# Kernel tuning notes

Measured on AMD Instinct MI355X. Metric: run time of the kernel, lower is better.

## Reference

```python
import jax, jax.numpy as jnp
import numpy as np

NU = 50000   # n_users
NI = 50000   # n_items
N = NU + NI  # total nodes in the square normalized adjacency
D = 64       # emb_dim
K = 4        # number of sub-graphs in hypergraph_list
E = 1000000  # interactions per sub-graph (symmetrized -> 2E nnz)


def setup_inputs() -> dict:
    key = jax.random.key(0)
    ks = jax.random.split(key, 9)
    stdv = 1.0 / np.sqrt(D)
    return {
        "x": jax.random.normal(ks[0], (N, D), jnp.float32),
        "hgc1_bias": jax.random.uniform(ks[1], (D,), jnp.float32, -stdv, stdv),
        "fc1_W": jax.random.normal(ks[2], (D, D), jnp.float32) * stdv,
        "fus_l1_W": jax.random.normal(ks[3], (D, D), jnp.float32) * stdv,
        "fus_l1_b": jnp.zeros((D,), jnp.float32),
        "fus_l2_W": jax.random.normal(ks[4], (1, D), jnp.float32) * stdv,
        "fus_l2_b": jnp.zeros((1,), jnp.float32),
        "rows": jax.random.randint(ks[5], (K, E), 0, NU),
        "cols": jax.random.randint(ks[6], (K, E), 0, NI),
    }


def reference(x, hgc1_bias, fc1_W, fus_l1_W, fus_l1_b, fus_l2_W, fus_l2_b, rows, cols):
    def spmm(src, dst, val, h):
        # (L @ h)[i] = sum over nnz (src=i): val * h[dst]
        return jax.ops.segment_sum(val[:, None] * h[dst], src, num_segments=N)

    def step(xc, rc):
        r, c = rc
        # symmetric bipartite adjacency A (items offset by NU)
        src = jnp.concatenate([r, c + NU])  # (2E,)
        dst = jnp.concatenate([c + NU, r])  # (2E,)
        # D^-1/2 A D^-1/2  (degree = row nnz count, as in (A>0).sum)
        deg = jax.ops.segment_sum(jnp.ones(src.shape, jnp.float32), src, num_segments=N) + 1e-7
        dinv = deg ** -0.5
        val = dinv[src] * dinv[dst]
        # HGNN2: relu -> hgc1 (bias add, edge=G^T x, x=G edge; G symmetric) -> softmax -> fc1
        h = jax.nn.relu(xc) + hgc1_bias
        edge = spmm(src, dst, val, h)
        node = spmm(src, dst, val, edge)
        node = jax.nn.softmax(node, axis=1)
        node = node @ fc1_W.T  # fc1 has no bias
        # Fusion gate (dropout off in eval)
        emb = jnp.stack([xc, node])  # (2, N, D)
        score = jax.nn.softmax(
            jnp.tanh(emb @ fus_l1_W.T + fus_l1_b) @ fus_l2_W.T + fus_l2_b, axis=0
        )  # (2, N, 1)
        x_new = jnp.sum(score * emb, axis=0)
        return x_new, (x_new, edge)

    _, (nodes, edges) = jax.lax.scan(step, x, (rows, cols))
    # embedding_list[sub_key] = [x, edge] per sub-graph -> stacked (K, N, D)
    return nodes, edges
```

## Files before the change

### kernel.cpp

```cpp
#include <hip/hip_runtime.h>
#include <hip/hip_bf16.h>

#define NU_ 50000
#define NI_ 50000
#define NN  (NU_ + NI_)
#define DD  64
#define KK  4
#define EE  1000000
#define SCAN_B ((NN + 255) / 256)

#define P_RANGES 8
#define RANGE_SZ ((NN + P_RANGES - 1) / P_RANGES)

__global__ void k_hist(const int* __restrict__ r, const int* __restrict__ c,
                       int* __restrict__ cnt) {
    int e = blockIdx.x * blockDim.x + threadIdx.x;
    if (e >= EE) return;
    int a = r[e], b = c[e];
    if ((unsigned)a >= (unsigned)NU_ || (unsigned)b >= (unsigned)NI_) return;
    atomicAdd(&cnt[a], 1);
    atomicAdd(&cnt[NU_ + b], 1);
}

__global__ __launch_bounds__(256) void k_bsum(const int* __restrict__ cnt,
                                              int* __restrict__ bsum) {
    __shared__ int s[256];
    int i = blockIdx.x * 256 + threadIdx.x;
    s[threadIdx.x] = (i < NN) ? cnt[i] : 0;
    __syncthreads();
    #pragma unroll
    for (int off = 128; off > 0; off >>= 1) {
        if (threadIdx.x < off) s[threadIdx.x] += s[threadIdx.x + off];
        __syncthreads();
    }
    if (threadIdx.x == 0) bsum[blockIdx.x] = s[0];
}

__global__ __launch_bounds__(512) void k_sscan(const int* __restrict__ bsum,
                                               int* __restrict__ bofs) {
    __shared__ int s[512];
    int tid = threadIdx.x;
    s[tid] = (tid < SCAN_B) ? bsum[tid] : 0;
    __syncthreads();
    #pragma unroll
    for (int off = 1; off < 512; off <<= 1) {
        int v = (tid >= off) ? s[tid - off] : 0;
        __syncthreads();
        s[tid] += v;
        __syncthreads();
    }
    if (tid < SCAN_B) bofs[tid] = (tid > 0) ? s[tid - 1] : 0;
}

__global__ __launch_bounds__(256) void k_apply(const int* __restrict__ cnt,
                                               const int* __restrict__ bofs,
                                               int* __restrict__ row_ptr,
                                               int* __restrict__ cursor,
                                               float* __restrict__ dinv) {
    __shared__ int s[256];
    int i = blockIdx.x * 256 + threadIdx.x;
    int v = (i < NN) ? cnt[i] : 0;
    s[threadIdx.x] = v;
    __syncthreads();
    #pragma unroll
    for (int off = 1; off < 256; off <<= 1) {
        int t = (threadIdx.x >= off) ? s[threadIdx.x - off] : 0;
        __syncthreads();
        s[threadIdx.x] += t;
        __syncthreads();
    }
    if (i < NN) {
        int incl = s[threadIdx.x] + bofs[blockIdx.x];
        int excl = incl - v;
        row_ptr[i] = excl;
        cursor[i] = excl;
        dinv[i] = rsqrtf((float)v + 1e-7f);
        if (i == NN - 1) row_ptr[NN] = incl;
    }
}

__global__ __launch_bounds__(256) void k_scatter2(const int* __restrict__ r,
                                                  const int* __restrict__ c,
                                                  int* __restrict__ cursor,
                                                  int* __restrict__ adj) {
    const int g = blockIdx.x;
    const int lo = g * RANGE_SZ;
    int e = blockIdx.y * 256 + threadIdx.x;
    if (e >= EE) return;
    int a = r[e], b = c[e];
    if ((unsigned)a >= (unsigned)NU_ || (unsigned)b >= (unsigned)NI_) return;
    b += NU_;
    if ((unsigned)(a - lo) < (unsigned)RANGE_SZ) {
        int p = atomicAdd(&cursor[a], 1);
        adj[p] = b;
    }
    if ((unsigned)(b - lo) < (unsigned)RANGE_SZ) {
        int q = atomicAdd(&cursor[b], 1);
        adj[q] = a;
    }
}

__global__ __launch_bounds__(256) void k_prep(const float* __restrict__ x,
                                              const float* __restrict__ bias,
                                              const float* __restrict__ dinv,
                                              float* __restrict__ hbuf,
                                              float* __restrict__ h2buf) {
    int i = blockIdx.x * 256 + threadIdx.x;
    int node = i >> 4;
    float dv = dinv[node];
    const float4 xv = ((const float4*)x)[i];
    const float4 bv = ((const float4*)bias)[i & 15];
    float4 o;
    o.x = dv * (fmaxf(xv.x, 0.f) + bv.x);
    o.y = dv * (fmaxf(xv.y, 0.f) + bv.y);
    o.z = dv * (fmaxf(xv.z, 0.f) + bv.z);
    o.w = dv * (fmaxf(xv.w, 0.f) + bv.w);
    ((float4*)hbuf)[i] = o;
    if (blockIdx.x == 0 && threadIdx.x < 32) {
        float4 z = {0.f, 0.f, 0.f, 0.f};
        if (threadIdx.x < 16)
            ((float4*)&hbuf[(size_t)NN * DD])[threadIdx.x] = z;
        else
            ((float4*)&h2buf[(size_t)NN * DD])[threadIdx.x - 16] = z;
    }
}

__global__ __launch_bounds__(256) void k_pullA(const int* __restrict__ row_ptr,
                                               const int* __restrict__ adj,
                                               const float* __restrict__ dinv,
                                               const float* __restrict__ hbuf,
                                               float* __restrict__ out_e,
                                               float* __restrict__ h2buf) {
    const int wave = threadIdx.x >> 6;
    const int lane = threadIdx.x & 63;
    const int sub  = lane >> 4;
    const int l16  = lane & 15;
    const int row  = (blockIdx.x * 4 + wave) * 4 + sub;
    const int start = row_ptr[row];
    const int end   = row_ptr[row + 1];
    float4 a0 = {0,0,0,0}, a1 = {0,0,0,0}, a2 = {0,0,0,0}, a3 = {0,0,0,0};
    for (int base = start; base < end; base += 16) {
        int t = base + l16;
        int idx = (t < end) ? adj[t] : NN;
        #pragma unroll
        for (int j = 0; j < 16; j++) {
            int nbr = __shfl(idx, (sub << 4) | j);
            const float4 hv = *(const float4*)&hbuf[(size_t)nbr * DD + l16 * 4];
            float4* ac = (j & 2) ? ((j & 1) ? &a3 : &a2) : ((j & 1) ? &a1 : &a0);
            ac->x += hv.x; ac->y += hv.y; ac->z += hv.z; ac->w += hv.w;
        }
    }
    float4 acc = {a0.x + a1.x + a2.x + a3.x, a0.y + a1.y + a2.y + a3.y,
                  a0.z + a1.z + a2.z + a3.z, a0.w + a1.w + a2.w + a3.w};
    const float dr = dinv[row];
    float4 e = {dr * acc.x, dr * acc.y, dr * acc.z, dr * acc.w};
    *(float4*)&out_e[(size_t)row * DD + l16 * 4] = e;
    float4 e2 = {dr * e.x, dr * e.y, dr * e.z, dr * e.w};
    *(float4*)&h2buf[(size_t)row * DD + l16 * 4] = e2;
}

__global__ __launch_bounds__(256) void k_pullB(const int* __restrict__ row_ptr,
                                               const int* __restrict__ adj,
                                               const float* __restrict__ dinv,
                                               const float* __restrict__ h2buf,
                                               float* __restrict__ out_n) {
    const int wave = threadIdx.x >> 6;
    const int lane = threadIdx.x & 63;
    const int sub  = lane >> 4;
    const int l16  = lane & 15;
    const int row  = (blockIdx.x * 4 + wave) * 4 + sub;
    const int start = row_ptr[row];
    const int end   = row_ptr[row + 1];
    float4 a0 = {0,0,0,0}, a1 = {0,0,0,0}, a2 = {0,0,0,0}, a3 = {0,0,0,0};
    for (int base = start; base < end; base += 16) {
        int t = base + l16;
        int idx = (t < end) ? adj[t] : NN;
        #pragma unroll
        for (int j = 0; j < 16; j++) {
            int nbr = __shfl(idx, (sub << 4) | j);
            const float4 hv = *(const float4*)&h2buf[(size_t)nbr * DD + l16 * 4];
            float4* ac = (j & 2) ? ((j & 1) ? &a3 : &a2) : ((j & 1) ? &a1 : &a0);
            ac->x += hv.x; ac->y += hv.y; ac->z += hv.z; ac->w += hv.w;
        }
    }
    float4 acc = {a0.x + a1.x + a2.x + a3.x, a0.y + a1.y + a2.y + a3.y,
                  a0.z + a1.z + a2.z + a3.z, a0.w + a1.w + a2.w + a3.w};
    const float dr = dinv[row];
    float4 o = {dr * acc.x, dr * acc.y, dr * acc.z, dr * acc.w};
    *(float4*)&out_n[(size_t)row * DD + l16 * 4] = o;
}

#define BC(v, d) __uint_as_float(__builtin_amdgcn_readlane(__float_as_uint(v), (d)))

__global__ __launch_bounds__(256) void k_row(
    const float* __restrict__ node, const float* __restrict__ xsrc,
    const float* __restrict__ fc1W, const float* __restrict__ fusW,
    const float* __restrict__ l1b, const float* __restrict__ l2w,
    const float* __restrict__ l2b, float* __restrict__ out_nodes) {
    const int wave = threadIdx.x >> 6;
    const int lane = threadIdx.x & 63;

    float wf[DD], wu[DD];
    #pragma unroll
    for (int d = 0; d < DD; d += 4) {
        *(float4*)&wf[d] = *(const float4*)&fc1W[(size_t)lane * DD + d];
        *(float4*)&wu[d] = *(const float4*)&fusW[(size_t)lane * DD + d];
    }
    const float b1v = l1b[lane];
    const float l2v = l2w[lane];
    const float b2v = l2b[0];

    for (int row = blockIdx.x * 4 + wave; row < NN; row += gridDim.x * 4) {
        const size_t base = (size_t)row * DD + lane;
        float v = node[base];
        float m = v;
        #pragma unroll
        for (int s = 1; s < 64; s <<= 1) m = fmaxf(m, __shfl_xor(m, s));
        float ev = __expf(v - m);
        float sum = ev;
        #pragma unroll
        for (int s = 1; s < 64; s <<= 1) sum += __shfl_xor(sum, s);
        float sm = ev / sum;
        float n0 = 0, n1 = 0, n2 = 0, n3 = 0;
        #pragma unroll
        for (int d = 0; d < DD; d += 4) {
            n0 = fmaf(BC(sm, d),     wf[d],     n0);
            n1 = fmaf(BC(sm, d + 1), wf[d + 1], n1);
            n2 = fmaf(BC(sm, d + 2), wf[d + 2], n2);
            n3 = fmaf(BC(sm, d + 3), wf[d + 3], n3);
        }
        float nf = (n0 + n1) + (n2 + n3);
        float xc = xsrc[base];
        float a0 = 0, a1 = 0, a2 = 0, a3 = 0;
        #pragma unroll
        for (int d = 0; d < DD; d += 4) {
            a0 = fmaf(BC(xc, d),     wu[d],     a0);
            a1 = fmaf(BC(xc, d + 1), wu[d + 1], a1);
            a2 = fmaf(BC(xc, d + 2), wu[d + 2], a2);
            a3 = fmaf(BC(xc, d + 3), wu[d + 3], a3);
        }
        float tt = tanhf(((a0 + a1) + (a2 + a3)) + b1v);
        float p = tt * l2v;
        #pragma unroll
        for (int s = 1; s < 64; s <<= 1) p += __shfl_xor(p, s);
        float s_x = p + b2v;
        a0 = 0; a1 = 0; a2 = 0; a3 = 0;
        #pragma unroll
        for (int d = 0; d < DD; d += 4) {
            a0 = fmaf(BC(nf, d),     wu[d],     a0);
            a1 = fmaf(BC(nf, d + 1), wu[d + 1], a1);
            a2 = fmaf(BC(nf, d + 2), wu[d + 2], a2);
            a3 = fmaf(BC(nf, d + 3), wu[d + 3], a3);
        }
        tt = tanhf(((a0 + a1) + (a2 + a3)) + b1v);
        p = tt * l2v;
        #pragma unroll
        for (int s = 1; s < 64; s <<= 1) p += __shfl_xor(p, s);
        float s_n = p + b2v;
        float mm = fmaxf(s_x, s_n);
        float e0 = __expf(s_x - mm), e1 = __expf(s_n - mm);
        float inv = 1.0f / (e0 + e1);
        float xn = (e0 * xc + e1 * nf) * inv;
        out_nodes[base] = xn;
    }
}

extern "C" void kernel_launch(void* const* d_in, const int* in_sizes, int n_in,
                              void* d_out, int out_size, void* d_ws, size_t ws_size,
                              hipStream_t stream) {
    const float* x    = (const float*)d_in[0];
    const float* b1   = (const float*)d_in[1];
    const float* fc1W = (const float*)d_in[2];
    const float* fusW = (const float*)d_in[3];
    const float* l1b  = (const float*)d_in[4];
    const float* l2w  = (const float*)d_in[5];
    const float* l2b  = (const float*)d_in[6];
    const int* rows = (const int*)d_in[7];
    const int* cols = (const int*)d_in[8];
    float* out = (float*)d_out;

    const int ND = NN * DD;

    float* hbuf    = (float*)d_ws;
    float* h2buf   = hbuf + (size_t)(NN + 1) * DD;
    float* dinv    = h2buf + (size_t)(NN + 1) * DD;
    int*   cnt     = (int*)(dinv + NN);
    int*   row_ptr = cnt + NN;
    int*   cursor  = row_ptr + NN + 1;
    int*   bsum    = cursor + NN;
    int*   bofs    = bsum + SCAN_B;
    int*   adj     = bofs + SCAN_B;

    for (int k = 0; k < KK; k++) {
        const int* r = rows + (size_t)k * EE;
        const int* c = cols + (size_t)k * EE;
        const float* xk = (k == 0) ? x : out + (size_t)(k - 1) * ND;
        float* out_n = out + (size_t)k * ND;
        float* out_e = out + (size_t)(KK + k) * ND;

        hipMemsetAsync(cnt, 0, NN * sizeof(int), stream);
        k_hist<<<(EE + 255) / 256, 256, 0, stream>>>(r, c, cnt);
        k_bsum<<<SCAN_B, 256, 0, stream>>>(cnt, bsum);
        k_sscan<<<1, 512, 0, stream>>>(bsum, bofs);
        k_apply<<<SCAN_B, 256, 0, stream>>>(cnt, bofs, row_ptr, cursor, dinv);
        {
            dim3 g(P_RANGES, (EE + 255) / 256);
            k_scatter2<<<g, 256, 0, stream>>>(r, c, cursor, adj);
        }

        k_prep<<<ND / 4 / 256, 256, 0, stream>>>(xk, b1, dinv, hbuf, h2buf);

        k_pullA<<<NN / 16, 256, 0, stream>>>(row_ptr, adj, dinv, hbuf, out_e, h2buf);

        k_pullB<<<NN / 16, 256, 0, stream>>>(row_ptr, adj, dinv, h2buf, out_n);

        k_row<<<1024, 256, 0, stream>>>(out_n, xk, fc1W, fusW, l1b, l2w, l2b, out_n);
    }
}
```

Measured before the change: 1.849 ms.

## Bucket rows by degree for load-balanced SpMM and partition histogram atomics

Adds a degree histogram, a scan over it, and a scatter that builds a permutation grouping rows of similar degree. Each 16-lane group in the pull kernels then processes rows of near-equal length, which reduces divergence within a wave. The pull inner loop now iterates over the actual neighbour count instead of always doing 16 padded gathers, so the dummy zero-row loads go away. The degree histogram kernel is also split into 8 node ranges, matching the scatter kernel, to improve atomic locality. The cost is three extra small kernels per sub-graph and scattered output rows due to the permuted row order.

```diff
diff --git a/kernel.cpp b/kernel.cpp
--- a/kernel.cpp
+++ b/kernel.cpp
@@ -12,14 +12,18 @@
 #define P_RANGES 8
 #define RANGE_SZ ((NN + P_RANGES - 1) / P_RANGES)
 
-__global__ void k_hist(const int* __restrict__ r, const int* __restrict__ c,
-                       int* __restrict__ cnt) {
-    int e = blockIdx.x * blockDim.x + threadIdx.x;
+__global__ __launch_bounds__(256) void k_hist2(const int* __restrict__ r,
+                                               const int* __restrict__ c,
+                                               int* __restrict__ cnt) {
+    const int g = blockIdx.x;
+    const int lo = g * RANGE_SZ;
+    int e = blockIdx.y * 256 + threadIdx.x;
     if (e >= EE) return;
     int a = r[e], b = c[e];
     if ((unsigned)a >= (unsigned)NU_ || (unsigned)b >= (unsigned)NI_) return;
-    atomicAdd(&cnt[a], 1);
-    atomicAdd(&cnt[NU_ + b], 1);
+    b += NU_;
+    if ((unsigned)(a - lo) < (unsigned)RANGE_SZ) atomicAdd(&cnt[a], 1);
+    if ((unsigned)(b - lo) < (unsigned)RANGE_SZ) atomicAdd(&cnt[b], 1);
 }
 
 __global__ __launch_bounds__(256) void k_bsum(const int* __restrict__ cnt,
@@ -37,9 +41,11 @@
 }
 
 __global__ __launch_bounds__(512) void k_sscan(const int* __restrict__ bsum,
-                                               int* __restrict__ bofs) {
+                                               int* __restrict__ bofs,
+                                               int* __restrict__ dhist) {
     __shared__ int s[512];
     int tid = threadIdx.x;
+    if (tid < 64) dhist[tid] = 0;
     s[tid] = (tid < SCAN_B) ? bsum[tid] : 0;
     __syncthreads();
     #pragma unroll
@@ -56,10 +62,13 @@
                                                const int* __restrict__ bofs,
                                                int* __restrict__ row_ptr,
                                                int* __restrict__ cursor,
-                                               float* __restrict__ dinv) {
+                                               float* __restrict__ dinv,
+                                               int* __restrict__ dhist) {
     __shared__ int s[256];
+    __shared__ int hs[64];
     int i = blockIdx.x * 256 + threadIdx.x;
     int v = (i < NN) ? cnt[i] : 0;
+    if (threadIdx.x < 64) hs[threadIdx.x] = 0;
     s[threadIdx.x] = v;
     __syncthreads();
     #pragma unroll
@@ -76,7 +85,34 @@
         cursor[i] = excl;
         dinv[i] = rsqrtf((float)v + 1e-7f);
         if (i == NN - 1) row_ptr[NN] = incl;
-    }
+        atomicAdd(&hs[v < 63 ? v : 63], 1);
+    }
+    __syncthreads();
+    if (threadIdx.x < 64 && hs[threadIdx.x] > 0)
+        atomicAdd(&dhist[threadIdx.x], hs[threadIdx.x]);
+}
+
+__global__ __launch_bounds__(64) void k_dscan(const int* __restrict__ dhist,
+                                              int* __restrict__ dofs) {
+    int lane = threadIdx.x;
+    int h = dhist[lane];
+    int v = h;
+    #pragma unroll
+    for (int off = 1; off < 64; off <<= 1) {
+        int u = __shfl_up(v, off);
+        if (lane >= off) v += u;
+    }
+    dofs[lane] = v - h;
+}
+
+__global__ __launch_bounds__(256) void k_dscat(const int* __restrict__ cnt,
+                                               int* __restrict__ dofs,
+                                               int* __restrict__ perm) {
+    int i = blockIdx.x * 256 + threadIdx.x;
+    if (i >= NN) return;
+    int b = cnt[i]; if (b > 63) b = 63;
+    int pos = atomicAdd(&dofs[b], 1);
+    perm[pos] = i;
 }
 
 __global__ __launch_bounds__(256) void k_scatter2(const int* __restrict__ r,
@@ -103,8 +139,7 @@
 __global__ __launch_bounds__(256) void k_prep(const float* __restrict__ x,
                                               const float* __restrict__ bias,
                                               const float* __restrict__ dinv,
-                                              float* __restrict__ hbuf,
-                                              float* __restrict__ h2buf) {
+                                              float* __restrict__ hbuf) {
     int i = blockIdx.x * 256 + threadIdx.x;
     int node = i >> 4;
     float dv = dinv[node];
@@ -116,17 +151,11 @@
     o.z = dv * (fmaxf(xv.z, 0.f) + bv.z);
     o.w = dv * (fmaxf(xv.w, 0.f) + bv.w);
     ((float4*)hbuf)[i] = o;
-    if (blockIdx.x == 0 && threadIdx.x < 32) {
-        float4 z = {0.f, 0.f, 0.f, 0.f};
-        if (threadIdx.x < 16)
-            ((float4*)&hbuf[(size_t)NN * DD])[threadIdx.x] = z;
-        else
-            ((float4*)&h2buf[(size_t)NN * DD])[threadIdx.x - 16] = z;
-    }
 }
 
 __global__ __launch_bounds__(256) void k_pullA(const int* __restrict__ row_ptr,
                                                const int* __restrict__ adj,
+                                               const int* __restrict__ perm,
                                                const float* __restrict__ dinv,
                                                const float* __restrict__ hbuf,
                                                float* __restrict__ out_e,
@@ -135,23 +164,37 @@
     const int lane = threadIdx.x & 63;
     const int sub  = lane >> 4;
     const int l16  = lane & 15;
-    const int row  = (blockIdx.x * 4 + wave) * 4 + sub;
+    const int lb   = sub << 4;
+    const int row  = perm[blockIdx.x * 16 + wave * 4 + sub];
     const int start = row_ptr[row];
     const int end   = row_ptr[row + 1];
-    float4 a0 = {0,0,0,0}, a1 = {0,0,0,0}, a2 = {0,0,0,0}, a3 = {0,0,0,0};
+    float4 aA = {0,0,0,0}, aB = {0,0,0,0};
     for (int base = start; base < end; base += 16) {
+        int n = end - base; if (n > 16) n = 16;
         int t = base + l16;
-        int idx = (t < end) ? adj[t] : NN;
-        #pragma unroll
-        for (int j = 0; j < 16; j++) {
-            int nbr = __shfl(idx, (sub << 4) | j);
-            const float4 hv = *(const float4*)&hbuf[(size_t)nbr * DD + l16 * 4];
-            float4* ac = (j & 2) ? ((j & 1) ? &a3 : &a2) : ((j & 1) ? &a1 : &a0);
-            ac->x += hv.x; ac->y += hv.y; ac->z += hv.z; ac->w += hv.w;
-        }
-    }
-    float4 acc = {a0.x + a1.x + a2.x + a3.x, a0.y + a1.y + a2.y + a3.y,
-                  a0.z + a1.z + a2.z + a3.z, a0.w + a1.w + a2.w + a3.w};
+        int idx = (l16 < n) ? adj[t] : 0;
+        int j = 0;
+        for (; j + 3 < n; j += 4) {
+            int n0 = __shfl(idx, lb | j);
+            int n1 = __shfl(idx, lb | (j + 1));
+            int n2 = __shfl(idx, lb | (j + 2));
+            int n3 = __shfl(idx, lb | (j + 3));
+            const float4 v0 = *(const float4*)&hbuf[(size_t)n0 * DD + l16 * 4];
+            const float4 v1 = *(const float4*)&hbuf[(size_t)n1 * DD + l16 * 4];
+            const float4 v2 = *(const float4*)&hbuf[(size_t)n2 * DD + l16 * 4];
+            const float4 v3 = *(const float4*)&hbuf[(size_t)n3 * DD + l16 * 4];
+            aA.x += v0.x; aA.y += v0.y; aA.z += v0.z; aA.w += v0.w;
+            aB.x += v1.x; aB.y += v1.y; aB.z += v1.z; aB.w += v1.w;
+            aA.x += v2.x; aA.y += v2.y; aA.z += v2.z; aA.w += v2.w;
+            aB.x += v3.x; aB.y += v3.y; aB.z += v3.z; aB.w += v3.w;
+        }
+        for (; j < n; j++) {
+            int nb = __shfl(idx, lb | j);
+            const float4 v = *(const float4*)&hbuf[(size_t)nb * DD + l16 * 4];
+            aA.x += v.x; aA.y += v.y; aA.z += v.z; aA.w += v.w;
+        }
+    }
+    float4 acc = {aA.x + aB.x, aA.y + aB.y, aA.z + aB.z, aA.w + aB.w};
     const float dr = dinv[row];
     float4 e = {dr * acc.x, dr * acc.y, dr * acc.z, dr * acc.w};
     *(float4*)&out_e[(size_t)row * DD + l16 * 4] = e;
@@ -161,6 +204,7 @@
 
 __global__ __launch_bounds__(256) void k_pullB(const int* __restrict__ row_ptr,
                                                const int* __restrict__ adj,
+                                               const int* __restrict__ perm,
                                                const float* __restrict__ dinv,
                                                const float* __restrict__ h2buf,
                                                float* __restrict__ out_n) {
@@ -168,23 +212,37 @@
     const int lane = threadIdx.x & 63;
     const int sub  = lane >> 4;
     const int l16  = lane & 15;
-    const int row  = (blockIdx.x * 4 + wave) * 4 + sub;
+    const int lb   = sub << 4;
+    const int row  = perm[blockIdx.x * 16 + wave * 4 + sub];
     const int start = row_ptr[row];
     const int end   = row_ptr[row + 1];
-    float4 a0 = {0,0,0,0}, a1 = {0,0,0,0}, a2 = {0,0,0,0}, a3 = {0,0,0,0};
+    float4 aA = {0,0,0,0}, aB = {0,0,0,0};
     for (int base = start; base < end; base += 16) {
+        int n = end - base; if (n > 16) n = 16;
         int t = base + l16;
-        int idx = (t < end) ? adj[t] : NN;
-        #pragma unroll
-        for (int j = 0; j < 16; j++) {
-            int nbr = __shfl(idx, (sub << 4) | j);
-            const float4 hv = *(const float4*)&h2buf[(size_t)nbr * DD + l16 * 4];
-            float4* ac = (j & 2) ? ((j & 1) ? &a3 : &a2) : ((j & 1) ? &a1 : &a0);
-            ac->x += hv.x; ac->y += hv.y; ac->z += hv.z; ac->w += hv.w;
-        }
-    }
-    float4 acc = {a0.x + a1.x + a2.x + a3.x, a0.y + a1.y + a2.y + a3.y,
-                  a0.z + a1.z + a2.z + a3.z, a0.w + a1.w + a2.w + a3.w};
+        int idx = (l16 < n) ? adj[t] : 0;
+        int j = 0;
+        for (; j + 3 < n; j += 4) {
+            int n0 = __shfl(idx, lb | j);
+            int n1 = __shfl(idx, lb | (j + 1));
+            int n2 = __shfl(idx, lb | (j + 2));
+            int n3 = __shfl(idx, lb | (j + 3));
+            const float4 v0 = *(const float4*)&h2buf[(size_t)n0 * DD + l16 * 4];
+            const float4 v1 = *(const float4*)&h2buf[(size_t)n1 * DD + l16 * 4];
+            const float4 v2 = *(const float4*)&h2buf[(size_t)n2 * DD + l16 * 4];
+            const float4 v3 = *(const float4*)&h2buf[(size_t)n3 * DD + l16 * 4];
+            aA.x += v0.x; aA.y += v0.y; aA.z += v0.z; aA.w += v0.w;
+            aB.x += v1.x; aB.y += v1.y; aB.z += v1.z; aB.w += v1.w;
+            aA.x += v2.x; aA.y += v2.y; aA.z += v2.z; aA.w += v2.w;
+            aB.x += v3.x; aB.y += v3.y; aB.z += v3.z; aB.w += v3.w;
+        }
+        for (; j < n; j++) {
+            int nb = __shfl(idx, lb | j);
+            const float4 v = *(const float4*)&h2buf[(size_t)nb * DD + l16 * 4];
+            aA.x += v.x; aA.y += v.y; aA.z += v.z; aA.w += v.w;
+        }
+    }
+    float4 acc = {aA.x + aB.x, aA.y + aB.y, aA.z + aB.z, aA.w + aB.w};
     const float dr = dinv[row];
     float4 o = {dr * acc.x, dr * acc.y, dr * acc.z, dr * acc.w};
     *(float4*)&out_n[(size_t)row * DD + l16 * 4] = o;
@@ -287,9 +345,12 @@
     int*   cnt     = (int*)(dinv + NN);
     int*   row_ptr = cnt + NN;
     int*   cursor  = row_ptr + NN + 1;
-    int*   bsum    = cursor + NN;
+    int*   perm    = cursor + NN;
+    int*   bsum    = perm + NN;
     int*   bofs    = bsum + SCAN_B;
-    int*   adj     = bofs + SCAN_B;
+    int*   dhist   = bofs + SCAN_B;
+    int*   dofs    = dhist + 64;
+    int*   adj     = dofs + 64;
 
     for (int k = 0; k < KK; k++) {
         const int* r = rows + (size_t)k * EE;
@@ -299,20 +360,25 @@
         float* out_e = out + (size_t)(KK + k) * ND;
 
         hipMemsetAsync(cnt, 0, NN * sizeof(int), stream);
-        k_hist<<<(EE + 255) / 256, 256, 0, stream>>>(r, c, cnt);
+        {
+            dim3 g(P_RANGES, (EE + 255) / 256);
+            k_hist2<<<g, 256, 0, stream>>>(r, c, cnt);
+        }
         k_bsum<<<SCAN_B, 256, 0, stream>>>(cnt, bsum);
-        k_sscan<<<1, 512, 0, stream>>>(bsum, bofs);
-        k_apply<<<SCAN_B, 256, 0, stream>>>(cnt, bofs, row_ptr, cursor, dinv);
+        k_sscan<<<1, 512, 0, stream>>>(bsum, bofs, dhist);
+        k_apply<<<SCAN_B, 256, 0, stream>>>(cnt, bofs, row_ptr, cursor, dinv, dhist);
+        k_dscan<<<1, 64, 0, stream>>>(dhist, dofs);
+        k_dscat<<<SCAN_B, 256, 0, stream>>>(cnt, dofs, perm);
         {
             dim3 g(P_RANGES, (EE + 255) / 256);
             k_scatter2<<<g, 256, 0, stream>>>(r, c, cursor, adj);
         }
 
-        k_prep<<<ND / 4 / 256, 256, 0, stream>>>(xk, b1, dinv, hbuf, h2buf);
-
-        k_pullA<<<NN / 16, 256, 0, stream>>>(row_ptr, adj, dinv, hbuf, out_e, h2buf);
-
-        k_pullB<<<NN / 16, 256, 0, stream>>>(row_ptr, adj, dinv, h2buf, out_n);
+        k_prep<<<ND / 4 / 256, 256, 0, stream>>>(xk, b1, dinv, hbuf);
+
+        k_pullA<<<NN / 16, 256, 0, stream>>>(row_ptr, adj, perm, dinv, hbuf, out_e, h2buf);
+
+        k_pullB<<<NN / 16, 256, 0, stream>>>(row_ptr, adj, perm, dinv, h2buf, out_n);
 
         k_row<<<1024, 256, 0, stream>>>(out_n, xk, fc1W, fusW, l1b, l2w, l2b, out_n);
     }
```

Result: slower. 3.023 ms (+63.5%).
